# Performance work log

Measured on AMD Instinct MI355X. Metric: run time of the kernel, lower is better.

## Reference

```python
import jax, jax.numpy as jnp
import numpy as np

N = 4096          # residues
D = 256           # local feature dim
FACTOR = 2
H = 8             # global heads
DF = D * FACTOR   # 512
DH = DF // H      # 64 per-head dim
NUM_CHAINS = 64
NUM_BATCHES = 8


def index_mean(x, idx, mask, num_segments):
    """Masked segment mean, gathered back to per-element shape.
    x: [N, ...], idx: [N] int, mask: broadcastable to x (0/1)."""
    m = mask.astype(x.dtype)
    xm = x * m
    s = jax.ops.segment_sum(xm, idx, num_segments=num_segments)
    c = jax.ops.segment_sum(jnp.broadcast_to(m, x.shape), idx, num_segments=num_segments)
    mean = s / jnp.maximum(c, 1e-6)
    return mean[idx]


def setup_inputs() -> dict:
    key = jax.random.key(0)
    ks = jax.random.split(key, 12)
    s_in = 1.0 / np.sqrt(D)
    s_mid = 1.0 / np.sqrt(2 * DF)
    return {
        "local": jax.random.normal(ks[0], (N, D), jnp.float32),
        "chain": jax.random.randint(ks[1], (N,), 0, NUM_CHAINS),
        "batch": jax.random.randint(ks[2], (N,), 0, NUM_BATCHES),
        "mask": jax.random.bernoulli(ks[3], 0.9, (N,)),
        "W_key": jax.random.normal(ks[4], (D, DF), jnp.float32) * s_in,
        "b_key": jnp.zeros((DF,), jnp.float32),
        "W_value": jax.random.normal(ks[5], (D, DF), jnp.float32) * s_in,
        "b_value": jnp.zeros((DF,), jnp.float32),
        "W_query": jax.random.normal(ks[6], (D, DF), jnp.float32) * s_in,
        "b_query": jnp.zeros((DF,), jnp.float32),
        "W_bias": jax.random.normal(ks[7], (D, 2 * DF), jnp.float32) * s_in,
        "b_bias": jnp.zeros((2 * DF,), jnp.float32),
        "W_out": jax.random.normal(ks[8], (2 * DF, D), jnp.float32) * s_mid,
    }


def reference(local, chain, batch, mask,
              W_key, b_key, W_value, b_value, W_query, b_query,
              W_bias, b_bias, W_out):
    n = local.shape[0]
    k = jax.nn.gelu(local @ W_key + b_key).reshape(n, H, DH)
    v = (local @ W_value + b_value).reshape(n, H, DH)
    q = jax.nn.gelu(local @ W_query + b_query).reshape(n, H, DH)

    bias = index_mean(local @ W_bias + b_bias, batch, mask[:, None], NUM_BATCHES)

    # outer product key (x) value: [N, H, DH, DH]
    ov = k[:, :, :, None] * v[:, :, None, :]
    m4 = mask[:, None, None, None]
    chain_op = index_mean(ov, chain, m4, NUM_CHAINS)
    batch_op = index_mean(ov, batch, m4, NUM_BATCHES)
    operation = jnp.concatenate((chain_op, batch_op), axis=-2)  # [N, H, 2*DH, DH]

    out = jnp.einsum('bhvk,bhk->bhv', operation, q).reshape(n, -1) + bias
    return out @ W_out
```

## Files before the change

kernel.cpp:

```cpp
#include <hip/hip_runtime.h>
#include <math.h>

#define NN 4096
#define DD 256
#define DFF 512
#define HH 8
#define DHH 64
#define CAP_C 256
#define CAP_B 1024

#define OFF_KB     0
#define OFF_VB     1048576
#define OFF_QB     2097152
#define OFF_ATTNB  3145728
#define OFF_LOCALB 5242880
#define OFF_BSUM   5767168
#define OFF_CNT    5775360
#define OFF_WQKVT  5775616
#define OFF_WOUTT  5972224
#define OFF_LISTS  6103296
#define OFF_LPART  6152448

typedef __attribute__((ext_vector_type(8))) short bf16x8;
typedef __attribute__((ext_vector_type(4))) float floatx4;

__device__ __forceinline__ float gelu_f(float x) {
    const float c = 0.7978845608028654f;
    float t = tanhf(c * (x + 0.044715f * x * x * x));
    return 0.5f * x * (1.0f + t);
}

__device__ __forceinline__ unsigned short f2b(float f) {
    union { float f; unsigned int u; } v; v.f = f;
    unsigned int r = (v.u + 0x7FFFu + ((v.u >> 16) & 1u)) >> 16;
    return (unsigned short)r;
}

__global__ __launch_bounds__(256) void prep_kernel(
    const float* __restrict__ local,
    const float* __restrict__ Wk, const float* __restrict__ Wv,
    const float* __restrict__ Wq, const float* __restrict__ Wout,
    const int* __restrict__ batch, const int* __restrict__ mask,
    unsigned short* __restrict__ Wqkvt, unsigned short* __restrict__ Woutt,
    unsigned short* __restrict__ localb,
    float* __restrict__ Lpart, float* __restrict__ zero_base)
{
    const int bid = blockIdx.x, tid = threadIdx.x;
    if (bid < 640) {
        const float* src; unsigned short* dst; int R, C, r0, c0;
        if (bid < 384) {
            int m = bid >> 7, ti = bid & 127;
            src = (m == 0) ? Wk : (m == 1) ? Wv : Wq;
            dst = Wqkvt + (size_t)m * 512 * 256;
            R = 256; C = 512;
            r0 = (ti >> 4) * 32; c0 = (ti & 15) * 32;
        } else {
            int ti = bid - 384;
            src = Wout; dst = Woutt;
            R = 1024; C = 256;
            r0 = (ti >> 3) * 32; c0 = (ti & 7) * 32;
        }
        __shared__ float Tl[32][33];
        int ty = tid >> 3, tx = tid & 7;
        float4 v = *(const float4*)(src + (size_t)(r0 + ty) * C + c0 + tx * 4);
        Tl[tx * 4 + 0][ty] = v.x;
        Tl[tx * 4 + 1][ty] = v.y;
        Tl[tx * 4 + 2][ty] = v.z;
        Tl[tx * 4 + 3][ty] = v.w;
        __syncthreads();
        ushort4 o;
        o.x = f2b(Tl[ty][tx * 4 + 0]);
        o.y = f2b(Tl[ty][tx * 4 + 1]);
        o.z = f2b(Tl[ty][tx * 4 + 2]);
        o.w = f2b(Tl[ty][tx * 4 + 3]);
        *(ushort4*)(dst + (size_t)(c0 + ty) * R + r0 + tx * 4) = o;
    } else if (bid < 704) {
        int p = bid - 640;
        float accl[8] = {};
        int n0 = p * 64;
        for (int r = 0; r < 64; ++r) {
            int n = n0 + r;
            float v = local[(size_t)n * DD + tid];
            int bb = batch[n];
            float vm = mask[n] ? v : 0.0f;
#pragma unroll
            for (int b = 0; b < 8; ++b)
                accl[b] += (bb == b) ? vm : 0.0f;
        }
#pragma unroll
        for (int b = 0; b < 8; ++b)
            Lpart[(size_t)p * 2048 + b * 256 + tid] = accl[b];
    } else if (bid < 1216) {
        int p = bid - 704;
        size_t base = (size_t)p * 2048 + tid * 8;
        float4 a0 = *(const float4*)(local + base);
        float4 a1 = *(const float4*)(local + base + 4);
        ushort4 p0, p1;
        p0.x = f2b(a0.x); p0.y = f2b(a0.y); p0.z = f2b(a0.z); p0.w = f2b(a0.w);
        p1.x = f2b(a1.x); p1.y = f2b(a1.y); p1.z = f2b(a1.z); p1.w = f2b(a1.w);
        *(ushort4*)(localb + base) = p0;
        *(ushort4*)(localb + base + 4) = p1;
    } else {
        float4 z4 = make_float4(0.f, 0.f, 0.f, 0.f);
        for (int i = tid; i < 2112; i += 256)
            ((float4*)zero_base)[i] = z4;
    }
}

__global__ __launch_bounds__(256) void qkv_kernel(
    const unsigned short* __restrict__ localb,
    const unsigned short* __restrict__ Wqkvt,
    const float* __restrict__ bk, const float* __restrict__ bv,
    const float* __restrict__ bq, unsigned short* __restrict__ KVQb,
    const int* __restrict__ chain, const int* __restrict__ batch,
    const int* __restrict__ mask, int* __restrict__ cnt,
    int* __restrict__ lists, const float* __restrict__ Lpart,
    const float* __restrict__ Wbias, float* __restrict__ Bsum)
{
    __shared__ __align__(16) char smem[36864];
    const int u = blockIdx.x, tid = threadIdx.x;
    int* cntc_m   = cnt;
    int* cntc_all = cnt + 64;
    int* cntb_m   = cnt + 128;
    int* cntb_all = cnt + 136;
    int* listc_m   = lists;
    int* listc_all = listc_m + 64 * CAP_C;
    int* listb_m   = listc_all + 64 * CAP_C;
    int* listb_all = listb_m + 8 * CAP_B;

    if (u < 384) {
        typedef unsigned short (*t72)[72];
        t72 Asl = (t72)smem;
        t72 Bsl = (t72)(smem + 18432);
        const int wave = tid >> 6, lane = tid & 63;
        const int kq = lane >> 4, la = lane & 15;
        const int cx = u % 12, ry = u / 12;
        const int row0 = ry * 128, cg0 = cx * 128;
        const int wrow = (wave & 1) * 64, wcol = (wave >> 1) * 64;

        floatx4 acc[4][4] = {};
        for (int kk = 0; kk < 256; kk += 64) {
#pragma unroll
            for (int t = 0; t < 4; ++t) {
                int idx = tid + t * 256;
                int rr = idx >> 3, kc = (idx & 7) * 8;
                *(float4*)&Asl[rr][kc] =
                    *(const float4*)(localb + (size_t)(row0 + rr) * DD + kk + kc);
                *(float4*)&Bsl[rr][kc] =
                    *(const float4*)(Wqkvt + (size_t)(cg0 + rr) * DD + kk + kc);
            }
            __syncthreads();
#pragma unroll
            for (int ks = 0; ks < 2; ++ks) {
                bf16x8 af[4], bf[4];
#pragma unroll
                for (int t = 0; t < 4; ++t) {
                    af[t] = *(const bf16x8*)&Asl[wrow + t * 16 + la][ks * 32 + kq * 8];
                    bf[t] = *(const bf16x8*)&Bsl[wcol + t * 16 + la][ks * 32 + kq * 8];
                }
#pragma unroll
                for (int at = 0; at < 4; ++at)
#pragma unroll
                    for (int ct = 0; ct < 4; ++ct)
                        acc[at][ct] = __builtin_amdgcn_mfma_f32_16x16x32_bf16(
                            af[at], bf[ct], acc[at][ct], 0, 0, 0);
            }
            __syncthreads();
        }
        const int sel = cg0 >> 9;
        const int do_gelu = (sel != 1);
        const float* bias = (sel == 0) ? bk : (sel == 1) ? bv : bq;
        unsigned short* C = KVQb + (size_t)sel * (NN * DFF);
#pragma unroll
        for (int ct = 0; ct < 4; ++ct) {
            int colw = (cg0 + wcol + ct * 16 + la) & 511;
            float bb = bias[colw];
#pragma unroll
            for (int at = 0; at < 4; ++at)
#pragma unroll
                for (int i = 0; i < 4; ++i) {
                    int row = row0 + wrow + at * 16 + kq * 4 + i;
                    float o = acc[at][ct][i] + bb;
                    if (do_gelu) o = gelu_f(o);
                    C[(size_t)row * DFF + colw] = f2b(o);
                }
        }
    } else if (u < 400) {
        int* sh = (int*)smem;
        int* hc_m = sh;        int* hc_all = sh + 64;
        int* hb_m = sh + 128;  int* hb_all = sh + 136;
        int* pc_m = sh + 144;  int* pc_all = sh + 208;
        int* pb_m = sh + 272;  int* pb_all = sh + 280;
        if (tid < 64) { hc_m[tid] = 0; hc_all[tid] = 0; }
        if (tid < 8)  { hb_m[tid] = 0; hb_all[tid] = 0; }
        __syncthreads();
        int n = (u - 384) * 256 + tid;
        int c = chain[n], b = batch[n], m = mask[n];
        int rc_all = atomicAdd(&hc_all[c], 1);
        int rb_all = atomicAdd(&hb_all[b], 1);
        int rc_m = -1, rb_m = -1;
        if (m) { rc_m = atomicAdd(&hc_m[c], 1); rb_m = atomicAdd(&hb_m[b], 1); }
        __syncthreads();
        if (tid < 64) {
            pc_all[tid] = atomicAdd(&cntc_all[tid], hc_all[tid]);
            pc_m[tid]   = atomicAdd(&cntc_m[tid],   hc_m[tid]);
        }
        if (tid < 8) {
            pb_all[tid] = atomicAdd(&cntb_all[tid], hb_all[tid]);
            pb_m[tid]   = atomicAdd(&cntb_m[tid],   hb_m[tid]);
        }
        __syncthreads();
        int ia = pc_all[c] + rc_all; if (ia < CAP_C) listc_all[c * CAP_C + ia] = n;
        int ib = pb_all[b] + rb_all; if (ib < CAP_B) listb_all[b * CAP_B + ib] = n;
        if (m) {
            int ja = pc_m[c] + rc_m; if (ja < CAP_C) listc_m[c * CAP_C + ja] = n;
            int jb = pb_m[b] + rb_m; if (jb < CAP_B) listb_m[b * CAP_B + jb] = n;
        }
    } else {
        int t = u - 400;
        const int seg = t >> 3, kz = t & 7;
        float (*Ltmp)[32] = (float(*)[32])smem;
        float* Lk = (float*)(smem + 8192);
        for (int idx = tid; idx < 2048; idx += 256) {
            int p = idx >> 5, k = idx & 31;
            Ltmp[p][k] = Lpart[(size_t)p * 2048 + seg * 256 + kz * 32 + k];
        }
        __syncthreads();
        if (tid < 32) {
            float s = 0.0f;
            for (int p = 0; p < 64; ++p) s += Ltmp[p][tid];
            Lk[tid] = s;
        }
        __syncthreads();
        float4 a4 = make_float4(0, 0, 0, 0);
        for (int k = 0; k < 32; ++k) {
            float l = Lk[k];
            float4 w = *(const float4*)(Wbias + (size_t)(kz * 32 + k) * 1024 + tid * 4);
            a4.x += l * w.x; a4.y += l * w.y; a4.z += l * w.z; a4.w += l * w.w;
        }
        float* o = Bsum + (size_t)seg * 1024 + tid * 4;
        atomicAdd(o + 0, a4.x); atomicAdd(o + 1, a4.y);
        atomicAdd(o + 2, a4.z); atomicAdd(o + 3, a4.w);
    }
}

__global__ __launch_bounds__(256) void midein_kernel(
    const unsigned short* __restrict__ Kb, const unsigned short* __restrict__ Vb,
    const unsigned short* __restrict__ Qb,
    const int* __restrict__ cnt, const int* __restrict__ lists,
    const int* __restrict__ batch,
    const float* __restrict__ Bsum, const float* __restrict__ b_bias,
    unsigned short* __restrict__ attnb)
{
    const int u = blockIdx.x, tid = threadIdx.x;
    const int* cntc_m   = cnt;
    const int* cntc_all = cnt + 64;
    const int* cntb_m   = cnt + 128;
    const int* cntb_all = cnt + 136;
    const int* listc_m   = lists;
    const int* listc_all = listc_m + 64 * CAP_C;
    const int* listb_m   = listc_all + 64 * CAP_C;
    const int* listb_all = listb_m + 8 * CAP_B;

    int seg, h, outoff, cap, rm, ra;
    const int* list_m; const int* list_a;
    if (u < 512) {
        seg = u >> 3; h = u & 7; outoff = 0; cap = CAP_C;
        list_m = listc_m; list_a = listc_all;
        rm = min(cntc_m[seg], CAP_C);
        ra = min(cntc_all[seg], CAP_C);
    } else {
        int t = u - 512;
        seg = t >> 3; h = t & 7; outoff = 64; cap = CAP_B;
        list_m = listb_m; list_a = listb_all;
        rm = min(cntb_m[seg], CAP_B);
        ra = min(cntb_all[seg], CAP_B);
    }
    float scaleS = 1.0f / fmaxf((float)rm, 1e-6f);

    __shared__ unsigned short Ktl[64][36];
    __shared__ unsigned short Vtl[64][36];
    __shared__ unsigned short Sbl[64][72];
    __shared__ unsigned short Qsl[64][72];
    __shared__ float Bf[8][64];
    __shared__ int nrow[64];
    __shared__ int nbb[64];

    const int wave = tid >> 6, lane = tid & 63;
    const int la = lane & 15, kq = lane >> 4;
    const int colbase = h * 128 + outoff;

    floatx4 acc4[4] = {};
    for (int g = 0; g < rm; g += 32) {
#pragma unroll
        for (int it = 0; it < 2; ++it) {
            int item = tid + it * 256;
            int nl = item & 31, aq = item >> 5;
            int gg = g + nl;
            ushort4 kz4 = make_ushort4(0, 0, 0, 0);
            ushort4 vz4 = make_ushort4(0, 0, 0, 0);
            if (gg < rm) {
                int nn = list_m[seg * cap + gg];
                kz4 = *(const ushort4*)(Kb + (size_t)nn * DFF + h * DHH + aq * 4);
                vz4 = *(const ushort4*)(Vb + (size_t)nn * DFF + h * DHH + aq * 4);
            }
            Ktl[aq * 4 + 0][nl] = kz4.x; Ktl[aq * 4 + 1][nl] = kz4.y;
            Ktl[aq * 4 + 2][nl] = kz4.z; Ktl[aq * 4 + 3][nl] = kz4.w;
            Vtl[aq * 4 + 0][nl] = vz4.x; Vtl[aq * 4 + 1][nl] = vz4.y;
            Vtl[aq * 4 + 2][nl] = vz4.z; Vtl[aq * 4 + 3][nl] = vz4.w;
        }
        __syncthreads();
        bf16x8 a = *(const bf16x8*)&Ktl[wave * 16 + la][kq * 8];
#pragma unroll
        for (int bt = 0; bt < 4; ++bt) {
            bf16x8 b = *(const bf16x8*)&Vtl[bt * 16 + la][kq * 8];
            acc4[bt] = __builtin_amdgcn_mfma_f32_16x16x32_bf16(a, b, acc4[bt], 0, 0, 0);
        }
        __syncthreads();
    }
#pragma unroll
    for (int bt = 0; bt < 4; ++bt)
#pragma unroll
        for (int rg = 0; rg < 4; ++rg) {
            int aa = wave * 16 + kq * 4 + rg;
            int bb2 = bt * 16 + la;
            Sbl[aa][bb2] = f2b(acc4[bt][rg] * scaleS);
        }
#pragma unroll
    for (int e = tid; e < 512; e += 256) {
        int bbq = e >> 6, j = e & 63;
        float cm = (float)min(cntb_m[bbq], CAP_B);
        float inv = 1.0f / fmaxf(cm, 1e-6f);
        int col = colbase + j;
        Bf[bbq][j] = (Bsum[(size_t)bbq * 1024 + col] + cm * b_bias[col]) * inv;
    }
    __syncthreads();

    for (int g = 0; g < ra; g += 64) {
        if (tid < 64) {
            int gg = g + tid;
            int n = (gg < ra) ? list_a[seg * cap + gg] : -1;
            nrow[tid] = n;
            nbb[tid] = (n >= 0) ? batch[n] : 0;
        }
        __syncthreads();
        {
            int row = tid & 63, pr = tid >> 6;
            int n = nrow[row];
            if (n >= 0) {
#pragma unroll
                for (int it = 0; it < 2; ++it) {
                    int off = (pr + it * 4) * 8;
                    *(float4*)&Qsl[row][off] =
                        *(const float4*)(Qb + (size_t)n * DFF + h * DHH + off);
                }
            }
        }
        __syncthreads();

        floatx4 acc[4] = {};
#pragma unroll
        for (int ks = 0; ks < 2; ++ks) {
            bf16x8 a = *(const bf16x8*)&Qsl[wave * 16 + la][ks * 32 + kq * 8];
#pragma unroll
            for (int ct = 0; ct < 4; ++ct) {
                bf16x8 b = *(const bf16x8*)&Sbl[ct * 16 + la][ks * 32 + kq * 8];
                acc[ct] = __builtin_amdgcn_mfma_f32_16x16x32_bf16(a, b, acc[ct], 0, 0, 0);
            }
        }
#pragma unroll
        for (int ct = 0; ct < 4; ++ct)
#pragma unroll
            for (int rg = 0; rg < 4; ++rg) {
                int rowl = wave * 16 + kq * 4 + rg;
                float bias = Bf[nbb[rowl]][ct * 16 + la];
                Qsl[rowl][ct * 16 + la] = f2b(acc[ct][rg] + bias);
            }
        __syncthreads();
        {
            int row = tid & 63, pr = tid >> 6;
            int n = nrow[row];
            if (n >= 0) {
#pragma unroll
                for (int it = 0; it < 2; ++it) {
                    int off = (pr + it * 4) * 8;
                    *(float4*)(attnb + (size_t)n * 1024 + colbase + off) =
                        *(const float4*)&Qsl[row][off];
                }
            }
        }
        __syncthreads();
    }
}

__global__ __launch_bounds__(256) void mfma_gemm_final(
    const unsigned short* __restrict__ A, const unsigned short* __restrict__ Bt,
    float* __restrict__ out)
{
    const int K = 1024;
    __shared__ unsigned short Asl[32][136];
    __shared__ unsigned short Bsl[64][136];
    const int tid = threadIdx.x;
    const int wave = tid >> 6, lane = tid & 63;
    const int q = lane >> 4, r = lane & 15;
    const int row0 = blockIdx.y * 32, cg0 = blockIdx.x * 64;
    const int wrow = (wave & 1) * 16, wcol = (wave >> 1) * 32;

    floatx4 acc[2] = {};
    for (int kk = 0; kk < K; kk += 128) {
#pragma unroll
        for (int t = 0; t < 2; ++t) {
            int idx = tid + t * 256;
            int rr = idx >> 4, kc = (idx & 15) * 8;
            *(float4*)&Asl[rr][kc] = *(const float4*)(A + (size_t)(row0 + rr) * K + kk + kc);
        }
#pragma unroll
        for (int t = 0; t < 4; ++t) {
            int idx = tid + t * 256;
            int rr = idx >> 4, kc = (idx & 15) * 8;
            *(float4*)&Bsl[rr][kc] = *(const float4*)(Bt + (size_t)(cg0 + rr) * K + kk + kc);
        }
        __syncthreads();
#pragma unroll
        for (int sub = 0; sub < 4; ++sub) {
            bf16x8 a = *(const bf16x8*)&Asl[wrow + r][sub * 32 + q * 8];
#pragma unroll
            for (int c = 0; c < 2; ++c) {
                bf16x8 b = *(const bf16x8*)&Bsl[wcol + c * 16 + r][sub * 32 + q * 8];
                acc[c] = __builtin_amdgcn_mfma_f32_16x16x32_bf16(a, b, acc[c], 0, 0, 0);
            }
        }
        __syncthreads();
    }
#pragma unroll
    for (int c = 0; c < 2; ++c) {
        int col = cg0 + wcol + c * 16 + r;
#pragma unroll
        for (int i = 0; i < 4; ++i) {
            int row = row0 + wrow + q * 4 + i;
            out[(size_t)row * DD + col] = acc[c][i];
        }
    }
}

extern "C" void kernel_launch(void* const* d_in, const int* in_sizes, int n_in,
                              void* d_out, int out_size, void* d_ws, size_t ws_size,
                              hipStream_t stream)
{
    const float* local   = (const float*)d_in[0];
    const int*   chain   = (const int*)d_in[1];
    const int*   batch   = (const int*)d_in[2];
    const int*   mask    = (const int*)d_in[3];
    const float* W_key   = (const float*)d_in[4];
    const float* b_key   = (const float*)d_in[5];
    const float* W_value = (const float*)d_in[6];
    const float* b_value = (const float*)d_in[7];
    const float* W_query = (const float*)d_in[8];
    const float* b_query = (const float*)d_in[9];
    const float* W_bias  = (const float*)d_in[10];
    const float* b_bias  = (const float*)d_in[11];
    const float* W_out   = (const float*)d_in[12];
    float* out = (float*)d_out;

    float* ws = (float*)d_ws;
    unsigned short* Kb     = (unsigned short*)(ws + OFF_KB);
    unsigned short* Vb     = (unsigned short*)(ws + OFF_VB);
    unsigned short* Qb     = (unsigned short*)(ws + OFF_QB);
    unsigned short* attnb  = (unsigned short*)(ws + OFF_ATTNB);
    unsigned short* localb = (unsigned short*)(ws + OFF_LOCALB);
    float* Bsum   = ws + OFF_BSUM;
    int*   cnt    = (int*)(ws + OFF_CNT);
    unsigned short* Wqkvt = (unsigned short*)(ws + OFF_WQKVT);
    unsigned short* Woutt = (unsigned short*)(ws + OFF_WOUTT);
    int*   lists  = (int*)(ws + OFF_LISTS);
    float* Lpart  = ws + OFF_LPART;

    dim3 blk(256);

    prep_kernel<<<dim3(1217), blk, 0, stream>>>(
        local, W_key, W_value, W_query, W_out, batch, mask,
        Wqkvt, Woutt, localb, Lpart, ws + OFF_BSUM);

    qkv_kernel<<<dim3(464), blk, 0, stream>>>(
        localb, Wqkvt, b_key, b_value, b_query, Kb,
        chain, batch, mask, cnt, lists, Lpart, W_bias, Bsum);

    midein_kernel<<<dim3(576), blk, 0, stream>>>(
        Kb, Vb, Qb, cnt, lists, batch, Bsum, b_bias, attnb);

    mfma_gemm_final<<<dim3(4, 128), blk, 0, stream>>>(attnb, Woutt, out);
}
```

Measured before the change: 162.7 us.

## Split fused segment kernel into partial outer-product sums and parallel einsum

```diff
diff --git a/kernel.cpp b/kernel.cpp
--- a/kernel.cpp
+++ b/kernel.cpp
@@ -14,12 +14,14 @@
 #define OFF_QB     2097152
 #define OFF_ATTNB  3145728
 #define OFF_LOCALB 5242880
-#define OFF_BSUM   5767168
-#define OFF_CNT    5775360
-#define OFF_WQKVT  5775616
-#define OFF_WOUTT  5972224
-#define OFF_LISTS  6103296
-#define OFF_LPART  6152448
+#define OFF_STC    5767168
+#define OFF_STBP   7864320
+#define OFF_BSUM   8912896
+#define OFF_CNT    8921088
+#define OFF_WQKVT  8921344
+#define OFF_WOUTT  9117952
+#define OFF_LISTS  9249024
+#define OFF_LPART  9298176
 
 typedef __attribute__((ext_vector_type(8))) short bf16x8;
 typedef __attribute__((ext_vector_type(4))) float floatx4;
@@ -244,54 +246,41 @@
     }
 }
 
-__global__ __launch_bounds__(256) void midein_kernel(
+__global__ __launch_bounds__(256) void mid_kernel(
     const unsigned short* __restrict__ Kb, const unsigned short* __restrict__ Vb,
-    const unsigned short* __restrict__ Qb,
     const int* __restrict__ cnt, const int* __restrict__ lists,
-    const int* __restrict__ batch,
-    const float* __restrict__ Bsum, const float* __restrict__ b_bias,
-    unsigned short* __restrict__ attnb)
+    float* __restrict__ STc, float* __restrict__ STbp)
 {
     const int u = blockIdx.x, tid = threadIdx.x;
-    const int* cntc_m   = cnt;
-    const int* cntc_all = cnt + 64;
-    const int* cntb_m   = cnt + 128;
-    const int* cntb_all = cnt + 136;
-    const int* listc_m   = lists;
-    const int* listc_all = listc_m + 64 * CAP_C;
-    const int* listb_m   = listc_all + 64 * CAP_C;
-    const int* listb_all = listb_m + 8 * CAP_B;
-
-    int seg, h, outoff, cap, rm, ra;
-    const int* list_m; const int* list_a;
+    const int* cntc_m = cnt;
+    const int* cntb_m = cnt + 128;
+    const int* listc_m = lists;
+    const int* listb_m = lists + 2 * 64 * CAP_C;
+
+    int seg, h, r0, r1, cap;
+    const int* list; float* ST;
     if (u < 512) {
-        seg = u >> 3; h = u & 7; outoff = 0; cap = CAP_C;
-        list_m = listc_m; list_a = listc_all;
-        rm = min(cntc_m[seg], CAP_C);
-        ra = min(cntc_all[seg], CAP_C);
+        seg = u >> 3; h = u & 7;
+        cap = CAP_C; list = listc_m;
+        r0 = 0; r1 = min(cntc_m[seg], CAP_C);
+        ST = STc + ((size_t)(seg * HH + h) << 12);
     } else {
         int t = u - 512;
-        seg = t >> 3; h = t & 7; outoff = 64; cap = CAP_B;
-        list_m = listb_m; list_a = listb_all;
-        rm = min(cntb_m[seg], CAP_B);
-        ra = min(cntb_all[seg], CAP_B);
-    }
-    float scaleS = 1.0f / fmaxf((float)rm, 1e-6f);
+        int z = t >> 6; seg = (t >> 3) & 7; h = t & 7;
+        cap = CAP_B; list = listb_m;
+        int c = min(cntb_m[seg], CAP_B);
+        int chunk = (c + 3) / 4;
+        r0 = z * chunk; r1 = min(c, r0 + chunk);
+        ST = STbp + (size_t)z * 262144 + ((size_t)(seg * HH + h) << 12);
+    }
 
     __shared__ unsigned short Ktl[64][36];
     __shared__ unsigned short Vtl[64][36];
-    __shared__ unsigned short Sbl[64][72];
-    __shared__ unsigned short Qsl[64][72];
-    __shared__ float Bf[8][64];
-    __shared__ int nrow[64];
-    __shared__ int nbb[64];
-
     const int wave = tid >> 6, lane = tid & 63;
     const int la = lane & 15, kq = lane >> 4;
-    const int colbase = h * 128 + outoff;
 
     floatx4 acc4[4] = {};
-    for (int g = 0; g < rm; g += 32) {
+    for (int g = r0; g < r1; g += 32) {
 #pragma unroll
         for (int it = 0; it < 2; ++it) {
             int item = tid + it * 256;
@@ -299,8 +288,8 @@
             int gg = g + nl;
             ushort4 kz4 = make_ushort4(0, 0, 0, 0);
             ushort4 vz4 = make_ushort4(0, 0, 0, 0);
-            if (gg < rm) {
-                int nn = list_m[seg * cap + gg];
+            if (gg < r1) {
+                int nn = list[seg * cap + gg];
                 kz4 = *(const ushort4*)(Kb + (size_t)nn * DFF + h * DHH + aq * 4);
                 vz4 = *(const ushort4*)(Vb + (size_t)nn * DFF + h * DHH + aq * 4);
             }
@@ -318,14 +307,86 @@
         }
         __syncthreads();
     }
+
 #pragma unroll
     for (int bt = 0; bt < 4; ++bt)
 #pragma unroll
         for (int rg = 0; rg < 4; ++rg) {
             int aa = wave * 16 + kq * 4 + rg;
             int bb2 = bt * 16 + la;
-            Sbl[aa][bb2] = f2b(acc4[bt][rg] * scaleS);
-        }
+            ST[aa * 64 + bb2] = acc4[bt][rg];
+        }
+}
+
+__global__ __launch_bounds__(256) void einsum_kernel(
+    const float* __restrict__ STc, const float* __restrict__ STbp,
+    const int* __restrict__ cnt, const int* __restrict__ lists,
+    const unsigned short* __restrict__ Qb, const int* __restrict__ batch,
+    const float* __restrict__ Bsum, const float* __restrict__ b_bias,
+    unsigned short* __restrict__ attnb)
+{
+    const int id = blockIdx.x, tid = threadIdx.x;
+    const int* cntc_m   = cnt;
+    const int* cntc_all = cnt + 64;
+    const int* cntb_m   = cnt + 128;
+    const int* cntb_all = cnt + 136;
+    const int* listc_all = lists + 64 * CAP_C;
+    const int* listb_all = lists + 2 * 64 * CAP_C + 8 * CAP_B;
+
+    int seg, h, outoff, cap, r0, r1;
+    const int* list;
+    float scaleS;
+    bool is_chain;
+    if (id < 512) {
+        seg = id >> 3; h = id & 7; outoff = 0;
+        list = listc_all; cap = CAP_C; is_chain = true;
+        scaleS = 1.0f / fmaxf((float)min(cntc_m[seg], CAP_C), 1e-6f);
+        r0 = 0; r1 = min(cntc_all[seg], CAP_C);
+    } else {
+        int t = id - 512;
+        seg = t >> 6; h = (t >> 3) & 7;
+        int z = t & 7;
+        outoff = 64;
+        list = listb_all; cap = CAP_B; is_chain = false;
+        scaleS = 1.0f / fmaxf((float)min(cntb_m[seg], CAP_B), 1e-6f);
+        int c = min(cntb_all[seg], CAP_B);
+        int chunk = (c + 7) / 8;
+        r0 = z * chunk; r1 = min(c, r0 + chunk);
+    }
+
+    __shared__ unsigned short Sbl[64][72];
+    __shared__ unsigned short Qsl[64][72];
+    __shared__ float Bf[8][64];
+    __shared__ int nrow[64];
+    __shared__ int nbb[64];
+
+    const int wave = tid >> 6, lane = tid & 63;
+    const int la = lane & 15, kq = lane >> 4;
+    const int colbase = h * 128 + outoff;
+
+#pragma unroll
+    for (int i = 0; i < 4; ++i) {
+        int e = tid + i * 256;
+        float4 v;
+        if (is_chain) {
+            v = *(const float4*)(STc + ((size_t)(seg * HH + h) << 12) + (size_t)e * 4);
+        } else {
+            const float* Sg = STbp + ((size_t)(seg * HH + h) << 12) + (size_t)e * 4;
+            float4 v0 = *(const float4*)(Sg);
+            float4 v1 = *(const float4*)(Sg + 262144);
+            float4 v2 = *(const float4*)(Sg + 524288);
+            float4 v3 = *(const float4*)(Sg + 786432);
+            v.x = v0.x + v1.x + v2.x + v3.x;
+            v.y = v0.y + v1.y + v2.y + v3.y;
+            v.z = v0.z + v1.z + v2.z + v3.z;
+            v.w = v0.w + v1.w + v2.w + v3.w;
+        }
+        int a = e >> 4, b = (e & 15) * 4;
+        ushort4 o;
+        o.x = f2b(v.x * scaleS); o.y = f2b(v.y * scaleS);
+        o.z = f2b(v.z * scaleS); o.w = f2b(v.w * scaleS);
+        *(ushort4*)&Sbl[a][b] = o;
+    }
 #pragma unroll
     for (int e = tid; e < 512; e += 256) {
         int bbq = e >> 6, j = e & 63;
@@ -336,10 +397,10 @@
     }
     __syncthreads();
 
-    for (int g = 0; g < ra; g += 64) {
+    for (int g = r0; g < r1; g += 64) {
         if (tid < 64) {
             int gg = g + tid;
-            int n = (gg < ra) ? list_a[seg * cap + gg] : -1;
+            int n = (gg < r1) ? list[seg * cap + gg] : -1;
             nrow[tid] = n;
             nbb[tid] = (n >= 0) ? batch[n] : 0;
         }
@@ -464,10 +525,11 @@
 
     float* ws = (float*)d_ws;
     unsigned short* Kb     = (unsigned short*)(ws + OFF_KB);
-    unsigned short* Vb     = (unsigned short*)(ws + OFF_VB);
     unsigned short* Qb     = (unsigned short*)(ws + OFF_QB);
     unsigned short* attnb  = (unsigned short*)(ws + OFF_ATTNB);
     unsigned short* localb = (unsigned short*)(ws + OFF_LOCALB);
+    float* STc    = ws + OFF_STC;
+    float* STbp   = ws + OFF_STBP;
     float* Bsum   = ws + OFF_BSUM;
     int*   cnt    = (int*)(ws + OFF_CNT);
     unsigned short* Wqkvt = (unsigned short*)(ws + OFF_WQKVT);
@@ -485,8 +547,11 @@
         localb, Wqkvt, b_key, b_value, b_query, Kb,
         chain, batch, mask, cnt, lists, Lpart, W_bias, Bsum);
 
-    midein_kernel<<<dim3(576), blk, 0, stream>>>(
-        Kb, Vb, Qb, cnt, lists, batch, Bsum, b_bias, attnb);
+    mid_kernel<<<dim3(768), blk, 0, stream>>>(
+        Kb, (const unsigned short*)(ws + OFF_VB), cnt, lists, STc, STbp);
+
+    einsum_kernel<<<dim3(1024), blk, 0, stream>>>(
+        STc, STbp, cnt, lists, Qb, batch, Bsum, b_bias, attnb);
 
     mfma_gemm_final<<<dim3(4, 128), blk, 0, stream>>>(attnb, Woutt, out);
 }
```

New measurement: 147.1 us. 9.6% less time.
